# Kernel tuning notes

Measured on AMD Instinct MI355X. Metric: run time of the kernel, lower is better.

## Reference

```python
import jax, jax.numpy as jnp
import numpy as np

DIM = 512
HEADS = 8
HEAD_DIM = DIM // HEADS

def setup_inputs() -> dict:
    key = jax.random.key(0)
    ks = jax.random.split(key, 5)
    s = 1.0 / np.sqrt(DIM)
    x = jax.random.normal(ks[0], (4, 2048, DIM), dtype=jnp.float32)
    w_qkv = jax.random.uniform(ks[1], (DIM, 3 * DIM), jnp.float32, -s, s)
    b_qkv = jax.random.uniform(ks[2], (3 * DIM,), jnp.float32, -s, s)
    w_out = jax.random.uniform(ks[3], (DIM, DIM), jnp.float32, -s, s)
    b_out = jax.random.uniform(ks[4], (DIM,), jnp.float32, -s, s)
    return {"x": x, "w_qkv": w_qkv, "b_qkv": b_qkv, "w_out": w_out, "b_out": b_out}

def reference(x, w_qkv, b_qkv, w_out, b_out):
    B, N, D = x.shape
    qkv = x @ w_qkv + b_qkv  # [B, N, 3D]
    qkv = qkv.reshape(B, N, 3, HEADS, HEAD_DIM).transpose(2, 0, 3, 1, 4)  # [3, B, H, N, hd]
    q, k, v = qkv[0], qkv[1], qkv[2]
    scale = 1.0 / np.sqrt(HEAD_DIM).astype(np.float32)
    attn = jnp.einsum('bhqd,bhkd->bhqk', q, k) * scale
    attn = jax.nn.softmax(attn, axis=-1)
    out = jnp.einsum('bhqk,bhkd->bhqd', attn, v)  # [B, H, N, hd]
    out = out.transpose(0, 2, 1, 3).reshape(B, N, D)
    return out @ w_out + b_out
```

## Files before the change

### kernel.cpp

```cpp
#include <hip/hip_runtime.h>

#define NB 4
#define NH 8
#define HD 64
#define DIMV 512
#define NSEQ 2048
#define QKVLD 1536
#define NTOK (NB*NSEQ)
#define KVB 64
#define QSCALE 0.18033688011112042f

typedef __attribute__((ext_vector_type(8))) short s8v;
typedef __attribute__((ext_vector_type(4))) float f4v;

typedef __attribute__((address_space(1))) void gvoid;
typedef __attribute__((address_space(3))) void lvoid;

__device__ __forceinline__ void load_lds16(const void* g, void* l){
  __builtin_amdgcn_global_load_lds((gvoid*)(void*)g, (lvoid*)l, 16, 0, 0);
}

__device__ __forceinline__ ushort f2bf(float f){
  unsigned u = __float_as_uint(f);
  u += 0x7fffu + ((u >> 16) & 1u);
  return (ushort)(u >> 16);
}

__device__ __forceinline__ unsigned pk2bf(float a, float b){
  return (unsigned)f2bf(a) | ((unsigned)f2bf(b) << 16);
}

__device__ __forceinline__ unsigned cvt_pk_bf16(float lo, float hi){
  unsigned r;
  asm("v_cvt_pk_bf16_f32 %0, %1, %2" : "=v"(r) : "v"(lo), "v"(hi));
  return r;
}
__device__ __forceinline__ float fexp2(float x){
  float r;
  asm("v_exp_f32 %0, %1" : "=v"(r) : "v"(x));
  return r;
}
__device__ __forceinline__ void plane32(unsigned &a, unsigned &b){
  asm("v_permlane32_swap_b32 %0, %1" : "+v"(a), "+v"(b));
}
__device__ __forceinline__ void plane16(unsigned &a, unsigned &b){
  asm("v_permlane16_swap_b32 %0, %1" : "+v"(a), "+v"(b));
}

__global__ __launch_bounds__(256) void k_prep(const float* __restrict__ x,
                                              ushort* __restrict__ xb,
                                              const float* __restrict__ w_qkv,
                                              ushort* __restrict__ wqkvT,
                                              const float* __restrict__ w_out,
                                              ushort* __restrict__ woutT){
  const int blk = blockIdx.x;
  const int tid = threadIdx.x;
  if (blk < 4096){
    const int i = blk * 256 + tid;
    float4 v = ((const float4*)x)[i];
    ushort4 o;
    o.x = f2bf(v.x); o.y = f2bf(v.y); o.z = f2bf(v.z); o.w = f2bf(v.w);
    ((ushort4*)xb)[i] = o;
    return;
  }
  __shared__ float t[32][33];
  const float* in; ushort* out; int C, bx, by;
  if (blk < 4864){
    const int idx = blk - 4096;
    in = w_qkv; out = wqkvT; C = QKVLD;
    bx = (idx % 48) * 32; by = (idx / 48) * 32;
  } else {
    const int idx = blk - 4864;
    in = w_out; out = woutT; C = DIMV;
    bx = (idx & 15) * 32; by = (idx >> 4) * 32;
  }
  const int tx = tid & 31, ty = tid >> 5;
  #pragma unroll
  for (int j = 0; j < 32; j += 8)
    t[ty + j][tx] = in[(size_t)(by + ty + j)*C + bx + tx];
  __syncthreads();
  #pragma unroll
  for (int j = 0; j < 32; j += 8)
    out[(size_t)(bx + ty + j)*DIMV + by + tx] = f2bf(t[tx][ty + j]);
}

template<int MODE, int NCT>
__global__ __launch_bounds__(256) void k_gemm(const ushort* __restrict__ A,
                                              const ushort* __restrict__ Bt,
                                              const float* __restrict__ bias,
                                              void* __restrict__ Cout,
                                              ushort* __restrict__ vtp,
                                              int N, int K){
  __shared__ ushort As[128*64];
  __shared__ ushort Bs[128*64];
  const int tid = threadIdx.x;
  const int w = tid >> 6, l = tid & 63;
  const int lr = l & 15, lg = l >> 4;
  const int wm = w >> 1, wn = w & 1;
  const int wg = blockIdx.x;
  const int xcd = wg & 7, idx = wg >> 3;
  const int tn = (idx % NCT) * 128;
  const int tm = (xcd * 8 + idx / NCT) * 128;
  const int r8 = l >> 3;
  const int lc = (l & 7) ^ r8;
  const int swz = (lr & 7) << 4;
  f4v acc[4][4] = {};

  for (int kk = 0; kk < K; kk += 64){
    __syncthreads();
    #pragma unroll
    for (int c = 0; c < 4; ++c){
      const int ci = w*4 + c;
      const int row = ci*8 + r8;
      load_lds16(A  + (size_t)(tm + row)*K + kk + lc*8, (char*)As + ci*1024);
      load_lds16(Bt + (size_t)(tn + row)*K + kk + lc*8, (char*)Bs + ci*1024);
    }
    __syncthreads();
    s8v af[4][2], bf[4][2];
    #pragma unroll
    for (int i = 0; i < 4; ++i){
      const int ra = (wm*64 + i*16 + lr)*128;
      const int rb = (wn*64 + i*16 + lr)*128;
      #pragma unroll
      for (int t = 0; t < 2; ++t){
        af[i][t] = *(const s8v*)((const char*)As + ra + ((t*64 + lg*16) ^ swz));
        bf[i][t] = *(const s8v*)((const char*)Bs + rb + ((t*64 + lg*16) ^ swz));
      }
    }
    #pragma unroll
    for (int mi = 0; mi < 4; ++mi)
      #pragma unroll
      for (int ni = 0; ni < 4; ++ni){
        acc[mi][ni] = __builtin_amdgcn_mfma_f32_16x16x32_bf16(af[mi][0], bf[ni][0], acc[mi][ni], 0, 0, 0);
        acc[mi][ni] = __builtin_amdgcn_mfma_f32_16x16x32_bf16(af[mi][1], bf[ni][1], acc[mi][ni], 0, 0, 0);
      }
  }

  if (MODE == 0){
    ushort* C = (ushort*)Cout;
    if (tn >= 2*DIMV){
      const int b = tm >> 11;
      const int n0 = (tm & (NSEQ-1)) + wm*64;
      #pragma unroll
      for (int ni = 0; ni < 4; ++ni){
        const int c = tn + wn*64 + ni*16 + lr;
        const int hd_i = c - 2*DIMV;
        const float bv = bias[c];
        ushort* vrow = vtp + ((size_t)(b*DIMV + hd_i))*NSEQ;
        #pragma unroll
        for (int mi = 0; mi < 4; ++mi){
          const int n = n0 + mi*16 + lg*4;
          uint2 pk;
          pk.x = pk2bf(acc[mi][ni][0] + bv, acc[mi][ni][1] + bv);
          pk.y = pk2bf(acc[mi][ni][2] + bv, acc[mi][ni][3] + bv);
          *(uint2*)(vrow + n) = pk;
        }
      }
    } else {
      #pragma unroll
      for (int ni = 0; ni < 4; ++ni){
        const int c = tn + wn*64 + ni*16 + lr;
        const float bv = bias[c];
        const float sc = (c < DIMV) ? QSCALE : 1.0f;
        #pragma unroll
        for (int mi = 0; mi < 4; ++mi)
          #pragma unroll
          for (int i = 0; i < 4; ++i){
            const int r = tm + wm*64 + mi*16 + lg*4 + i;
            C[(size_t)r*N + c] = f2bf((acc[mi][ni][i] + bv) * sc);
          }
      }
    }
  } else {
    float* C = (float*)Cout;
    #pragma unroll
    for (int ni = 0; ni < 4; ++ni){
      const int c = tn + wn*64 + ni*16 + lr;
      const float bv = bias[c];
      #pragma unroll
      for (int mi = 0; mi < 4; ++mi)
        #pragma unroll
        for (int i = 0; i < 4; ++i){
          const int r = tm + wm*64 + mi*16 + lg*4 + i;
          C[(size_t)r*N + c] = acc[mi][ni][i] + bv;
        }
    }
  }
}

__global__ __launch_bounds__(256, 2) void k_attn(const ushort* __restrict__ qkv,
                                                 const ushort* __restrict__ vt,
                                                 ushort* __restrict__ ao){
  __shared__ alignas(1024) char smem[2][16384];
  const int tid = threadIdx.x;
  const int w = tid >> 6, l = tid & 63;
  const int lr = l & 15, lg = l >> 4;
  const int wg = blockIdx.x;
  const int n = (wg & 7) * 64 + (wg >> 3);
  const int bh = n >> 4, xt = n & 15;
  const int b = bh >> 3, h = bh & 7;
  const int q0 = xt * 128 + w * 32;

  const ushort* qpA = qkv + (size_t)(b*NSEQ + q0 + lr)*QKVLD + h*HD + lg*8;
  const ushort* qpB = qpA + (size_t)16*QKVLD;
  const s8v qfA0 = *(const s8v*)(qpA);
  const s8v qfA1 = *(const s8v*)(qpA + 32);
  const s8v qfB0 = *(const s8v*)(qpB);
  const s8v qfB1 = *(const s8v*)(qpB + 32);

  const int r8 = l >> 3;
  const int lc = (l & 7) ^ r8;
  const int wbase = w * 16;
  const ushort* kg0 = qkv + (size_t)(b*NSEQ + wbase + r8)*QKVLD + DIMV + h*HD + lc*8;
  const ushort* kg1 = kg0 + (size_t)8*QKVLD;
  const ushort* vg0 = vt + (size_t)(bh*HD + wbase + r8)*NSEQ + lc*8;
  const ushort* vg1 = vg0 + (size_t)8*NSEQ;

  float lsumA = 0.0f, lsumB = 0.0f;
  f4v oA[4] = {}, oB[4] = {};

  load_lds16(kg0, &smem[0][ wbase   *128]);
  load_lds16(kg1, &smem[0][(wbase+8)*128]);
  load_lds16(vg0, &smem[0][ wbase   *128 + 8192]);
  load_lds16(vg1, &smem[0][(wbase+8)*128 + 8192]);
  kg0 += (size_t)KVB*QKVLD; kg1 += (size_t)KVB*QKVLD; vg0 += KVB; vg1 += KVB;

  const int swz = (lr & 7) << 4;
  const int ro0 = lr*128 + ((     lg*16) ^ swz);
  const int ro1 = lr*128 + ((64 + lg*16) ^ swz);

  for (int kt = 0; kt < NSEQ/KVB; ++kt){
    const int cur = kt & 1;
    __syncthreads();

    if (kt + 1 < NSEQ/KVB){
      char* dst = &smem[cur^1][0];
      load_lds16(kg0, dst +  wbase   *128);
      load_lds16(kg1, dst + (wbase+8)*128);
      load_lds16(vg0, dst +  wbase   *128 + 8192);
      load_lds16(vg1, dst + (wbase+8)*128 + 8192);
      kg0 += (size_t)KVB*QKVLD; kg1 += (size_t)KVB*QKVLD; vg0 += KVB; vg1 += KVB;
    }

    const char* b0 = &smem[cur][0] + ro0;
    const char* b1 = &smem[cur][0] + ro1;

    f4v sA[4] = {}, sB[4] = {};
    __builtin_amdgcn_s_setprio(1);
    #pragma unroll
    for (int kb = 0; kb < 4; ++kb){
      const s8v kf0 = *(const s8v*)(b0 + kb*2048);
      const s8v kf1 = *(const s8v*)(b1 + kb*2048);
      sA[kb] = __builtin_amdgcn_mfma_f32_16x16x32_bf16(kf0, qfA0, sA[kb], 0,0,0);
      sA[kb] = __builtin_amdgcn_mfma_f32_16x16x32_bf16(kf1, qfA1, sA[kb], 0,0,0);
      sB[kb] = __builtin_amdgcn_mfma_f32_16x16x32_bf16(kf0, qfB0, sB[kb], 0,0,0);
      sB[kb] = __builtin_amdgcn_mfma_f32_16x16x32_bf16(kf1, qfB1, sB[kb], 0,0,0);
    }
    __builtin_amdgcn_s_setprio(0);

    union { uint4 u; s8v v; } pfA0, pfA1, pfB0, pfB1;
    {
      const float p0 = fexp2(sA[0][0]), p1 = fexp2(sA[0][1]);
      const float p2 = fexp2(sA[0][2]), p3 = fexp2(sA[0][3]);
      const float p4 = fexp2(sA[1][0]), p5 = fexp2(sA[1][1]);
      const float p6 = fexp2(sA[1][2]), p7 = fexp2(sA[1][3]);
      lsumA += ((p0 + p1) + (p2 + p3)) + ((p4 + p5) + (p6 + p7));
      unsigned a = cvt_pk_bf16(p0, p1), bq = cvt_pk_bf16(p4, p5);
      plane32(a, bq); plane16(a, bq);
      unsigned c = cvt_pk_bf16(p2, p3), d = cvt_pk_bf16(p6, p7);
      plane32(c, d);  plane16(c, d);
      pfA0.u.x = a; pfA0.u.y = c; pfA0.u.z = bq; pfA0.u.w = d;
    }
    {
      const float p0 = fexp2(sA[2][0]), p1 = fexp2(sA[2][1]);
      const float p2 = fexp2(sA[2][2]), p3 = fexp2(sA[2][3]);
      const float p4 = fexp2(sA[3][0]), p5 = fexp2(sA[3][1]);
      const float p6 = fexp2(sA[3][2]), p7 = fexp2(sA[3][3]);
      lsumA += ((p0 + p1) + (p2 + p3)) + ((p4 + p5) + (p6 + p7));
      unsigned a = cvt_pk_bf16(p0, p1), bq = cvt_pk_bf16(p4, p5);
      plane32(a, bq); plane16(a, bq);
      unsigned c = cvt_pk_bf16(p2, p3), d = cvt_pk_bf16(p6, p7);
      plane32(c, d);  plane16(c, d);
      pfA1.u.x = a; pfA1.u.y = c; pfA1.u.z = bq; pfA1.u.w = d;
    }
    {
      const float p0 = fexp2(sB[0][0]), p1 = fexp2(sB[0][1]);
      const float p2 = fexp2(sB[0][2]), p3 = fexp2(sB[0][3]);
      const float p4 = fexp2(sB[1][0]), p5 = fexp2(sB[1][1]);
      const float p6 = fexp2(sB[1][2]), p7 = fexp2(sB[1][3]);
      lsumB += ((p0 + p1) + (p2 + p3)) + ((p4 + p5) + (p6 + p7));
      unsigned a = cvt_pk_bf16(p0, p1), bq = cvt_pk_bf16(p4, p5);
      plane32(a, bq); plane16(a, bq);
      unsigned c = cvt_pk_bf16(p2, p3), d = cvt_pk_bf16(p6, p7);
      plane32(c, d);  plane16(c, d);
      pfB0.u.x = a; pfB0.u.y = c; pfB0.u.z = bq; pfB0.u.w = d;
    }
    {
      const float p0 = fexp2(sB[2][0]), p1 = fexp2(sB[2][1]);
      const float p2 = fexp2(sB[2][2]), p3 = fexp2(sB[2][3]);
      const float p4 = fexp2(sB[3][0]), p5 = fexp2(sB[3][1]);
      const float p6 = fexp2(sB[3][2]), p7 = fexp2(sB[3][3]);
      lsumB += ((p0 + p1) + (p2 + p3)) + ((p4 + p5) + (p6 + p7));
      unsigned a = cvt_pk_bf16(p0, p1), bq = cvt_pk_bf16(p4, p5);
      plane32(a, bq); plane16(a, bq);
      unsigned c = cvt_pk_bf16(p2, p3), d = cvt_pk_bf16(p6, p7);
      plane32(c, d);  plane16(c, d);
      pfB1.u.x = a; pfB1.u.y = c; pfB1.u.z = bq; pfB1.u.w = d;
    }

    __builtin_amdgcn_s_setprio(1);
    #pragma unroll
    for (int ni = 0; ni < 4; ++ni){
      const s8v vf0 = *(const s8v*)(b0 + 8192 + ni*2048);
      const s8v vf1 = *(const s8v*)(b1 + 8192 + ni*2048);
      oA[ni] = __builtin_amdgcn_mfma_f32_16x16x32_bf16(vf0, pfA0.v, oA[ni], 0,0,0);
      oA[ni] = __builtin_amdgcn_mfma_f32_16x16x32_bf16(vf1, pfA1.v, oA[ni], 0,0,0);
      oB[ni] = __builtin_amdgcn_mfma_f32_16x16x32_bf16(vf0, pfB0.v, oB[ni], 0,0,0);
      oB[ni] = __builtin_amdgcn_mfma_f32_16x16x32_bf16(vf1, pfB1.v, oB[ni], 0,0,0);
    }
    __builtin_amdgcn_s_setprio(0);
  }

  float ltA = lsumA;
  ltA += __shfl_xor(ltA, 16, 64);
  ltA += __shfl_xor(ltA, 32, 64);
  float ltB = lsumB;
  ltB += __shfl_xor(ltB, 16, 64);
  ltB += __shfl_xor(ltB, 32, 64);
  const float invA = 1.0f / ltA;
  const float invB = 1.0f / ltB;
  ushort* opA = ao + (size_t)(b*NSEQ + q0 + lr)*DIMV + h*HD;
  ushort* opB = opA + (size_t)16*DIMV;
  #pragma unroll
  for (int ni = 0; ni < 4; ++ni){
    uint2 pk;
    pk.x = cvt_pk_bf16(oA[ni][0]*invA, oA[ni][1]*invA);
    pk.y = cvt_pk_bf16(oA[ni][2]*invA, oA[ni][3]*invA);
    *(uint2*)(opA + ni*16 + lg*4) = pk;
    pk.x = cvt_pk_bf16(oB[ni][0]*invB, oB[ni][1]*invB);
    pk.y = cvt_pk_bf16(oB[ni][2]*invB, oB[ni][3]*invB);
    *(uint2*)(opB + ni*16 + lg*4) = pk;
  }
}


extern "C" void kernel_launch(void* const* d_in, const int* in_sizes, int n_in,
                              void* d_out, int out_size, void* d_ws, size_t ws_size,
                              hipStream_t stream) {
  (void)in_sizes; (void)n_in; (void)out_size; (void)ws_size;
  const float* x     = (const float*)d_in[0];
  const float* w_qkv = (const float*)d_in[1];
  const float* b_qkv = (const float*)d_in[2];
  const float* w_out = (const float*)d_in[3];
  const float* b_out = (const float*)d_in[4];
  float* out = (float*)d_out;

  char* ws = (char*)d_ws;
  ushort* xb    = (ushort*)(ws);
  ushort* wqkvT = (ushort*)(ws + 8388608);
  ushort* woutT = (ushort*)(ws + 8388608 + 1572864);
  ushort* qkv   = (ushort*)(ws + 10485760);
  ushort* vt    = (ushort*)(ws + 35651584);
  ushort* ao    = (ushort*)(ws + 44040192);

  k_prep<<<dim3(4096 + 768 + 256), 256, 0, stream>>>(x, xb, w_qkv, wqkvT, w_out, woutT);
  k_gemm<0,12><<<dim3(768), 256, 0, stream>>>(xb, wqkvT, b_qkv, qkv, vt, QKVLD, DIMV);
  k_attn<<<dim3(512), 256, 0, stream>>>(qkv, vt, ao);
  k_gemm<1,4><<<dim3(256), 256, 0, stream>>>(ao, woutT, b_out, out, nullptr, DIMV, DIMV);
}
```

Measured before the change: 89.87 us.

## Halve attention block size and vectorize GEMM epilogue stores via swapped MFMA operands

The attention kernel now launches 1024 blocks of 128 threads (2 waves, 64 query rows each) instead of 512 blocks of 256 threads, so each wave loads a larger share of every K/V tile. This is meant to improve occupancy and load balance across the CUs. The GEMM swaps the MFMA operand order for the Q/K and output tiles so each lane holds four consecutive columns, which lets the epilogue write packed uint2 and float4 stores and read the bias as a float4 instead of issuing scalar strided stores. The V-transpose path keeps the original operand order. The risks are more K/V reload traffic per query row in attention and the extra code from two instantiations of the GEMM loop.

```diff
diff --git a/kernel.cpp b/kernel.cpp
--- a/kernel.cpp
+++ b/kernel.cpp
@@ -82,6 +82,53 @@
   #pragma unroll
   for (int j = 0; j < 32; j += 8)
     out[(size_t)(bx + ty + j)*DIMV + by + tx] = f2bf(t[tx][ty + j]);
+}
+
+template<bool SWAP>
+__device__ __forceinline__ void gemm_kloop(const ushort* __restrict__ A,
+                                           const ushort* __restrict__ Bt,
+                                           ushort* As, ushort* Bs,
+                                           int tm, int tn, int K,
+                                           int w, int l, int lr, int lg,
+                                           f4v acc[4][4]){
+  const int r8 = l >> 3;
+  const int lc = (l & 7) ^ r8;
+  const int swz = (lr & 7) << 4;
+  for (int kk = 0; kk < K; kk += 64){
+    __syncthreads();
+    #pragma unroll
+    for (int c = 0; c < 4; ++c){
+      const int ci = w*4 + c;
+      const int row = ci*8 + r8;
+      load_lds16(A  + (size_t)(tm + row)*K + kk + lc*8, (char*)As + ci*1024);
+      load_lds16(Bt + (size_t)(tn + row)*K + kk + lc*8, (char*)Bs + ci*1024);
+    }
+    __syncthreads();
+    const int wm = (w >> 1), wn = (w & 1);
+    s8v af[4][2], bf[4][2];
+    #pragma unroll
+    for (int i = 0; i < 4; ++i){
+      const int ra = (wm*64 + i*16 + lr)*128;
+      const int rb = (wn*64 + i*16 + lr)*128;
+      #pragma unroll
+      for (int t = 0; t < 2; ++t){
+        af[i][t] = *(const s8v*)((const char*)As + ra + ((t*64 + lg*16) ^ swz));
+        bf[i][t] = *(const s8v*)((const char*)Bs + rb + ((t*64 + lg*16) ^ swz));
+      }
+    }
+    #pragma unroll
+    for (int mi = 0; mi < 4; ++mi)
+      #pragma unroll
+      for (int ni = 0; ni < 4; ++ni){
+        if (SWAP){
+          acc[mi][ni] = __builtin_amdgcn_mfma_f32_16x16x32_bf16(bf[ni][0], af[mi][0], acc[mi][ni], 0, 0, 0);
+          acc[mi][ni] = __builtin_amdgcn_mfma_f32_16x16x32_bf16(bf[ni][1], af[mi][1], acc[mi][ni], 0, 0, 0);
+        } else {
+          acc[mi][ni] = __builtin_amdgcn_mfma_f32_16x16x32_bf16(af[mi][0], bf[ni][0], acc[mi][ni], 0, 0, 0);
+          acc[mi][ni] = __builtin_amdgcn_mfma_f32_16x16x32_bf16(af[mi][1], bf[ni][1], acc[mi][ni], 0, 0, 0);
+        }
+      }
+  }
 }
 
 template<int MODE, int NCT>
@@ -101,94 +148,69 @@
   const int xcd = wg & 7, idx = wg >> 3;
   const int tn = (idx % NCT) * 128;
   const int tm = (xcd * 8 + idx / NCT) * 128;
-  const int r8 = l >> 3;
-  const int lc = (l & 7) ^ r8;
-  const int swz = (lr & 7) << 4;
   f4v acc[4][4] = {};
 
-  for (int kk = 0; kk < K; kk += 64){
-    __syncthreads();
-    #pragma unroll
-    for (int c = 0; c < 4; ++c){
-      const int ci = w*4 + c;
-      const int row = ci*8 + r8;
-      load_lds16(A  + (size_t)(tm + row)*K + kk + lc*8, (char*)As + ci*1024);
-      load_lds16(Bt + (size_t)(tn + row)*K + kk + lc*8, (char*)Bs + ci*1024);
-    }
-    __syncthreads();
-    s8v af[4][2], bf[4][2];
-    #pragma unroll
-    for (int i = 0; i < 4; ++i){
-      const int ra = (wm*64 + i*16 + lr)*128;
-      const int rb = (wn*64 + i*16 + lr)*128;
-      #pragma unroll
-      for (int t = 0; t < 2; ++t){
-        af[i][t] = *(const s8v*)((const char*)As + ra + ((t*64 + lg*16) ^ swz));
-        bf[i][t] = *(const s8v*)((const char*)Bs + rb + ((t*64 + lg*16) ^ swz));
-      }
-    }
-    #pragma unroll
-    for (int mi = 0; mi < 4; ++mi)
-      #pragma unroll
-      for (int ni = 0; ni < 4; ++ni){
-        acc[mi][ni] = __builtin_amdgcn_mfma_f32_16x16x32_bf16(af[mi][0], bf[ni][0], acc[mi][ni], 0, 0, 0);
-        acc[mi][ni] = __builtin_amdgcn_mfma_f32_16x16x32_bf16(af[mi][1], bf[ni][1], acc[mi][ni], 0, 0, 0);
-      }
-  }
+  if (MODE == 0 && tn >= 2*DIMV){
+    gemm_kloop<false>(A, Bt, As, Bs, tm, tn, K, w, l, lr, lg, acc);
+    const int b = tm >> 11;
+    const int n0 = (tm & (NSEQ-1)) + wm*64;
+    #pragma unroll
+    for (int ni = 0; ni < 4; ++ni){
+      const int c = tn + wn*64 + ni*16 + lr;
+      const int hd_i = c - 2*DIMV;
+      const float bv = bias[c];
+      ushort* vrow = vtp + ((size_t)(b*DIMV + hd_i))*NSEQ;
+      #pragma unroll
+      for (int mi = 0; mi < 4; ++mi){
+        const int n = n0 + mi*16 + lg*4;
+        uint2 pk;
+        pk.x = pk2bf(acc[mi][ni][0] + bv, acc[mi][ni][1] + bv);
+        pk.y = pk2bf(acc[mi][ni][2] + bv, acc[mi][ni][3] + bv);
+        *(uint2*)(vrow + n) = pk;
+      }
+    }
+    return;
+  }
+
+  gemm_kloop<true>(A, Bt, As, Bs, tm, tn, K, w, l, lr, lg, acc);
 
   if (MODE == 0){
     ushort* C = (ushort*)Cout;
-    if (tn >= 2*DIMV){
-      const int b = tm >> 11;
-      const int n0 = (tm & (NSEQ-1)) + wm*64;
-      #pragma unroll
-      for (int ni = 0; ni < 4; ++ni){
-        const int c = tn + wn*64 + ni*16 + lr;
-        const int hd_i = c - 2*DIMV;
-        const float bv = bias[c];
-        ushort* vrow = vtp + ((size_t)(b*DIMV + hd_i))*NSEQ;
-        #pragma unroll
-        for (int mi = 0; mi < 4; ++mi){
-          const int n = n0 + mi*16 + lg*4;
-          uint2 pk;
-          pk.x = pk2bf(acc[mi][ni][0] + bv, acc[mi][ni][1] + bv);
-          pk.y = pk2bf(acc[mi][ni][2] + bv, acc[mi][ni][3] + bv);
-          *(uint2*)(vrow + n) = pk;
-        }
-      }
-    } else {
-      #pragma unroll
-      for (int ni = 0; ni < 4; ++ni){
-        const int c = tn + wn*64 + ni*16 + lr;
-        const float bv = bias[c];
-        const float sc = (c < DIMV) ? QSCALE : 1.0f;
-        #pragma unroll
-        for (int mi = 0; mi < 4; ++mi)
-          #pragma unroll
-          for (int i = 0; i < 4; ++i){
-            const int r = tm + wm*64 + mi*16 + lg*4 + i;
-            C[(size_t)r*N + c] = f2bf((acc[mi][ni][i] + bv) * sc);
-          }
+    const float sc = (tn < DIMV) ? QSCALE : 1.0f;
+    #pragma unroll
+    for (int ni = 0; ni < 4; ++ni){
+      const int c0 = tn + wn*64 + ni*16 + lg*4;
+      const float4 bv = *(const float4*)(bias + c0);
+      #pragma unroll
+      for (int mi = 0; mi < 4; ++mi){
+        const int r = tm + wm*64 + mi*16 + lr;
+        uint2 pk;
+        pk.x = pk2bf((acc[mi][ni][0] + bv.x)*sc, (acc[mi][ni][1] + bv.y)*sc);
+        pk.y = pk2bf((acc[mi][ni][2] + bv.z)*sc, (acc[mi][ni][3] + bv.w)*sc);
+        *(uint2*)(C + (size_t)r*N + c0) = pk;
       }
     }
   } else {
     float* C = (float*)Cout;
     #pragma unroll
     for (int ni = 0; ni < 4; ++ni){
-      const int c = tn + wn*64 + ni*16 + lr;
-      const float bv = bias[c];
-      #pragma unroll
-      for (int mi = 0; mi < 4; ++mi)
-        #pragma unroll
-        for (int i = 0; i < 4; ++i){
-          const int r = tm + wm*64 + mi*16 + lg*4 + i;
-          C[(size_t)r*N + c] = acc[mi][ni][i] + bv;
-        }
-    }
-  }
-}
-
-__global__ __launch_bounds__(256, 2) void k_attn(const ushort* __restrict__ qkv,
+      const int c0 = tn + wn*64 + ni*16 + lg*4;
+      const float4 bv = *(const float4*)(bias + c0);
+      #pragma unroll
+      for (int mi = 0; mi < 4; ++mi){
+        const int r = tm + wm*64 + mi*16 + lr;
+        float4 st;
+        st.x = acc[mi][ni][0] + bv.x;
+        st.y = acc[mi][ni][1] + bv.y;
+        st.z = acc[mi][ni][2] + bv.z;
+        st.w = acc[mi][ni][3] + bv.w;
+        *(float4*)(C + (size_t)r*N + c0) = st;
+      }
+    }
+  }
+}
+
+__global__ __launch_bounds__(128, 2) void k_attn(const ushort* __restrict__ qkv,
                                                  const ushort* __restrict__ vt,
                                                  ushort* __restrict__ ao){
   __shared__ alignas(1024) char smem[2][16384];
@@ -196,10 +218,10 @@
   const int w = tid >> 6, l = tid & 63;
   const int lr = l & 15, lg = l >> 4;
   const int wg = blockIdx.x;
-  const int n = (wg & 7) * 64 + (wg >> 3);
-  const int bh = n >> 4, xt = n & 15;
+  const int n = (wg & 7) * 128 + (wg >> 3);
+  const int bh = n >> 5, xt = n & 31;
   const int b = bh >> 3, h = bh & 7;
-  const int q0 = xt * 128 + w * 32;
+  const int q0 = xt * 64 + w * 32;
 
   const ushort* qpA = qkv + (size_t)(b*NSEQ + q0 + lr)*QKVLD + h*HD + lg*8;
   const ushort* qpB = qpA + (size_t)16*QKVLD;
@@ -210,20 +232,19 @@
 
   const int r8 = l >> 3;
   const int lc = (l & 7) ^ r8;
-  const int wbase = w * 16;
+  const int wbase = w * 32;
   const ushort* kg0 = qkv + (size_t)(b*NSEQ + wbase + r8)*QKVLD + DIMV + h*HD + lc*8;
-  const ushort* kg1 = kg0 + (size_t)8*QKVLD;
   const ushort* vg0 = vt + (size_t)(bh*HD + wbase + r8)*NSEQ + lc*8;
-  const ushort* vg1 = vg0 + (size_t)8*NSEQ;
 
   float lsumA = 0.0f, lsumB = 0.0f;
   f4v oA[4] = {}, oB[4] = {};
 
-  load_lds16(kg0, &smem[0][ wbase   *128]);
-  load_lds16(kg1, &smem[0][(wbase+8)*128]);
-  load_lds16(vg0, &smem[0][ wbase   *128 + 8192]);
-  load_lds16(vg1, &smem[0][(wbase+8)*128 + 8192]);
-  kg0 += (size_t)KVB*QKVLD; kg1 += (size_t)KVB*QKVLD; vg0 += KVB; vg1 += KVB;
+  #pragma unroll
+  for (int c = 0; c < 4; ++c){
+    load_lds16(kg0 + (size_t)(8*c)*QKVLD, &smem[0][(wbase + 8*c)*128]);
+    load_lds16(vg0 + (size_t)(8*c)*NSEQ,  &smem[0][(wbase + 8*c)*128 + 8192]);
+  }
+  kg0 += (size_t)KVB*QKVLD; vg0 += KVB;
 
   const int swz = (lr & 7) << 4;
   const int ro0 = lr*128 + ((     lg*16) ^ swz);
@@ -235,11 +256,12 @@
 
     if (kt + 1 < NSEQ/KVB){
       char* dst = &smem[cur^1][0];
-      load_lds16(kg0, dst +  wbase   *128);
-      load_lds16(kg1, dst + (wbase+8)*128);
-      load_lds16(vg0, dst +  wbase   *128 + 8192);
-      load_lds16(vg1, dst + (wbase+8)*128 + 8192);
-      kg0 += (size_t)KVB*QKVLD; kg1 += (size_t)KVB*QKVLD; vg0 += KVB; vg1 += KVB;
+      #pragma unroll
+      for (int c = 0; c < 4; ++c){
+        load_lds16(kg0 + (size_t)(8*c)*QKVLD, dst + (wbase + 8*c)*128);
+        load_lds16(vg0 + (size_t)(8*c)*NSEQ,  dst + (wbase + 8*c)*128 + 8192);
+      }
+      kg0 += (size_t)KVB*QKVLD; vg0 += KVB;
     }
 
     const char* b0 = &smem[cur][0] + ro0;
@@ -365,6 +387,6 @@
 
   k_prep<<<dim3(4096 + 768 + 256), 256, 0, stream>>>(x, xb, w_qkv, wqkvT, w_out, woutT);
   k_gemm<0,12><<<dim3(768), 256, 0, stream>>>(xb, wqkvT, b_qkv, qkv, vt, QKVLD, DIMV);
-  k_attn<<<dim3(512), 256, 0, stream>>>(qkv, vt, ao);
+  k_attn<<<dim3(1024), 128, 0, stream>>>(qkv, vt, ao);
   k_gemm<1,4><<<dim3(256), 256, 0, stream>>>(ao, woutT, b_out, out, nullptr, DIMV, DIMV);
 }
```

New measurement: 104.2 us. 16.0% more time.
